# Kernel tuning notes

Measured on AMD Instinct MI355X. Metric: run time of the kernel, lower is better.

## Reference

```python
import jax, jax.numpy as jnp
import numpy as np

HIDDEN = 1024
HEADS = 16
HEAD_DIM = HIDDEN // HEADS
B, S = 2, 2048


def setup_inputs() -> dict:
    key = jax.random.key(0)
    ks = jax.random.split(key, 9)
    sc = 1.0 / np.sqrt(HIDDEN)
    return {
        "hidden_state": jax.random.normal(ks[0], (B, S, HIDDEN), dtype=jnp.float32),
        "wq": jax.random.normal(ks[1], (HIDDEN, HIDDEN), dtype=jnp.float32) * sc,
        "bq": jax.random.normal(ks[2], (HIDDEN,), dtype=jnp.float32) * 0.01,
        "wk": jax.random.normal(ks[3], (HIDDEN, HIDDEN), dtype=jnp.float32) * sc,
        "bk": jax.random.normal(ks[4], (HIDDEN,), dtype=jnp.float32) * 0.01,
        "wv": jax.random.normal(ks[5], (HIDDEN, HIDDEN), dtype=jnp.float32) * sc,
        "bv": jax.random.normal(ks[6], (HIDDEN,), dtype=jnp.float32) * 0.01,
        "wo": jax.random.normal(ks[7], (HIDDEN, HIDDEN), dtype=jnp.float32) * sc,
        "bo": jax.random.normal(ks[8], (HIDDEN,), dtype=jnp.float32) * 0.01,
    }


def reference(hidden_state, wq, bq, wk, bk, wv, bv, wo, bo):
    b, s, _ = hidden_state.shape

    def split_head(x):  # [B,S,H*D] -> [B,H,S,D]
        return x.reshape(b, s, HEADS, HEAD_DIM).transpose(0, 2, 1, 3)

    q = split_head(hidden_state @ wq + bq)
    k = split_head(hidden_state @ wk + bk)
    v = split_head(hidden_state @ wv + bv)

    # NOTE: original scales by sqrt(hidden_size), NOT sqrt(head_dim)
    scale = 1.0 / jnp.sqrt(jnp.float32(HIDDEN))
    scores = jnp.einsum("bhqd,bhkd->bhqk", q, k) * scale  # [B,H,S,S]
    probs = jax.nn.softmax(scores, axis=-1)
    out = jnp.einsum("bhqk,bhkd->bhqd", probs, v)  # [B,H,S,D]

    # Faithful to source: transpose(-1,-2) then view (this is the original's
    # layout, which differs from the conventional transpose(1,2) merge)
    out = out.transpose(0, 1, 3, 2).reshape(b, -1, HEADS * HEAD_DIM)
    return out @ wo + bo
```

## Files before the change

kernel.cpp:

```cpp
#include <hip/hip_runtime.h>
#include <stdint.h>


typedef unsigned short u16;
typedef __bf16 bf16x8 __attribute__((ext_vector_type(8)));
typedef u16 u16x8 __attribute__((ext_vector_type(8)));
typedef u16 u16x4 __attribute__((ext_vector_type(4)));
typedef float f32x4 __attribute__((ext_vector_type(4)));

#define DEV static __device__ __forceinline__

DEV bf16x8 as_bf16x8(u16x8 u) { union { u16x8 u; bf16x8 b; } c; c.u = u; return c.b; }
DEV u16 f2bf(float f) {
  uint32_t u = __float_as_uint(f);
  u += 0x7fffu + ((u >> 16) & 1u);
  return (u16)(u >> 16);
}
#if __has_builtin(__builtin_amdgcn_exp2f)
DEV float ex2(float x) { return __builtin_amdgcn_exp2f(x); }
#else
DEV float ex2(float x) { return exp2f(x); }
#endif

DEV void gll16(const u16* g, u16* lds) {
  __builtin_amdgcn_global_load_lds((const __attribute__((address_space(1))) void*)g,
                                   (__attribute__((address_space(3))) void*)lds,
                                   16, 0, 0);
}

__global__ __launch_bounds__(256) void prep_kernel(
    const float* __restrict__ hid, const float* __restrict__ w0,
    const float* __restrict__ w1, const float* __restrict__ w2,
    const float* __restrict__ w3, u16* __restrict__ Ah,
    u16* __restrict__ Wt) {
  __shared__ __align__(16) float T[64][68];
  int bid = blockIdx.x, t = threadIdx.x;
  if (bid < 2048) {
    int i = (bid * 256 + t) * 8;
    f32x4 a = *(const f32x4*)&hid[i];
    f32x4 b = *(const f32x4*)&hid[i + 4];
    u16x8 o;
#pragma unroll
    for (int j = 0; j < 4; ++j) { o[j] = f2bf(a[j]); o[j + 4] = f2bf(b[j]); }
    *(u16x8*)&Ah[i] = o;
    return;
  }
  int tb = bid - 2048;
  int z = tb >> 8, rem = tb & 255;
  const float* W = (z == 0) ? w0 : (z == 1) ? w1 : (z == 2) ? w2 : w3;
  u16* O = Wt + (size_t)z * 1024 * 1024;
  int r0 = (rem >> 4) * 64, c0 = (rem & 15) * 64;
  int i = t >> 2, js = (t & 3) * 16;
#pragma unroll
  for (int jj = 0; jj < 16; jj += 4)
    *(f32x4*)&T[i][js + jj] = *(const f32x4*)&W[(size_t)(r0 + i) * 1024 + c0 + js + jj];
  __syncthreads();
#pragma unroll
  for (int seg = 0; seg < 2; ++seg) {
    u16x8 v;
#pragma unroll
    for (int jj = 0; jj < 8; ++jj) v[jj] = f2bf(T[js + seg * 8 + jj][i]);
    *(u16x8*)&O[(size_t)(c0 + i) * 1024 + r0 + js + seg * 8] = v;
  }
}

DEV void gemm_body(const u16* __restrict__ A, const u16* __restrict__ Bt,
                   const float* __restrict__ bias, u16* __restrict__ C,
                   int mode, float scale) {
  __shared__ __align__(16) u16 As[2][128 * 32], Bs[2][128 * 32];
  int tid = threadIdx.x, lane = tid & 63, w = tid >> 6;
  int quad = lane >> 4, l15 = lane & 15;
  int m0 = blockIdx.x * 128, n0 = blockIdx.y * 128;
  int wm = w >> 1, wn = w & 1;
  f32x4 acc[4][4] = {};

  const int idx0 = tid, idx1 = 256 + tid;
  const int row0 = idx0 >> 2, c0g = ((idx0 & 3) ^ ((row0 >> 1) & 3)) * 8;
  const int row1 = idx1 >> 2, c1g = ((idx1 & 3) ^ ((row1 >> 1) & 3)) * 8;
  const u16* Ap0 = A + (size_t)(m0 + row0) * 1024 + c0g;
  const u16* Ap1 = A + (size_t)(m0 + row1) * 1024 + c1g;
  const u16* Bp0 = Bt + (size_t)(n0 + row0) * 1024 + c0g;
  const u16* Bp1 = Bt + (size_t)(n0 + row1) * 1024 + c1g;

  u16x8 ta0, ta1, tb0, tb1;
  ta0 = *(const u16x8*)Ap0;
  ta1 = *(const u16x8*)Ap1;
  tb0 = *(const u16x8*)Bp0;
  tb1 = *(const u16x8*)Bp1;
  *(u16x8*)&As[0][idx0 * 8] = ta0;
  *(u16x8*)&As[0][idx1 * 8] = ta1;
  *(u16x8*)&Bs[0][idx0 * 8] = tb0;
  *(u16x8*)&Bs[0][idx1 * 8] = tb1;
  __syncthreads();

  for (int k0 = 0; k0 < 1024; k0 += 32) {
    int cur = (k0 >> 5) & 1;
    if (k0 < 992) {
      ta0 = *(const u16x8*)(Ap0 + k0 + 32);
      ta1 = *(const u16x8*)(Ap1 + k0 + 32);
      tb0 = *(const u16x8*)(Bp0 + k0 + 32);
      tb1 = *(const u16x8*)(Bp1 + k0 + 32);
    }

    bf16x8 af[4], bfr[4];
#pragma unroll
    for (int mt = 0; mt < 4; ++mt) {
      int row = wm * 64 + mt * 16 + l15;
      af[mt] = as_bf16x8(*(const u16x8*)&As[cur][row * 32 + (quad ^ ((row >> 1) & 3)) * 8]);
    }
#pragma unroll
    for (int nt = 0; nt < 4; ++nt) {
      int row = wn * 64 + nt * 16 + l15;
      bfr[nt] = as_bf16x8(*(const u16x8*)&Bs[cur][row * 32 + (quad ^ ((row >> 1) & 3)) * 8]);
    }
    __builtin_amdgcn_s_setprio(1);
#pragma unroll
    for (int mt = 0; mt < 4; ++mt)
#pragma unroll
      for (int nt = 0; nt < 4; ++nt)
        acc[mt][nt] = __builtin_amdgcn_mfma_f32_16x16x32_bf16(af[mt], bfr[nt], acc[mt][nt], 0, 0, 0);
    __builtin_amdgcn_s_setprio(0);

    if (k0 < 992) {
      int nb = cur ^ 1;
      *(u16x8*)&As[nb][idx0 * 8] = ta0;
      *(u16x8*)&As[nb][idx1 * 8] = ta1;
      *(u16x8*)&Bs[nb][idx0 * 8] = tb0;
      *(u16x8*)&Bs[nb][idx1 * 8] = tb1;
    }
    __syncthreads();
  }

#pragma unroll
  for (int nt = 0; nt < 4; ++nt) {
    int n = n0 + wn * 64 + nt * 16 + l15;
    float bv = bias[n];
#pragma unroll
    for (int mt = 0; mt < 4; ++mt) {
      int mbase = m0 + wm * 64 + mt * 16 + quad * 4;
      if (mode == 2) {
        int b = mbase >> 11, s = mbase & 2047, h = n >> 6, d = n & 63;
        size_t base = (((size_t)(b * 16 + h)) * 64 + d) * 2048 + s;
        u16x4 pk;
#pragma unroll
        for (int r = 0; r < 4; ++r) pk[r] = f2bf((acc[mt][nt][r] + bv) * scale);
        *(u16x4*)&C[base] = pk;
      } else {
#pragma unroll
        for (int r = 0; r < 4; ++r) {
          int m = mbase + r;
          int b = m >> 11, s = m & 2047, h = n >> 6, d = n & 63;
          C[(((size_t)(b * 16 + h)) * 2048 + s) * 64 + d] =
              f2bf((acc[mt][nt][r] + bv) * scale);
        }
      }
    }
  }
}

__global__ __launch_bounds__(256) void qkv_gemm(
    const u16* __restrict__ A, const u16* __restrict__ Wt,
    const float* __restrict__ bq, const float* __restrict__ bk,
    const float* __restrict__ bv, u16* __restrict__ Qb, u16* __restrict__ Kb,
    u16* __restrict__ Vt) {
  int z = blockIdx.z;
  const u16* Bt = Wt + (size_t)z * 1024 * 1024;
  const float* bias = (z == 0) ? bq : (z == 1) ? bk : bv;
  u16* C = (z == 0) ? Qb : (z == 1) ? Kb : Vt;
  gemm_body(A, Bt, bias, C, (z == 2) ? 2 : 1, (z == 0) ? 0.045084220f : 1.0f);
}

__global__ __launch_bounds__(256) void out_gemm(
    const u16* __restrict__ A, const u16* __restrict__ Wt,
    const float* __restrict__ bo, float* __restrict__ C) {
  const u16* Bt = Wt + (size_t)3 * 1024 * 1024;
  __shared__ __align__(16) u16 As[2][64 * 32], Bs[2][128 * 32];
  int tid = threadIdx.x, lane = tid & 63, w = tid >> 6;
  int quad = lane >> 4, l15 = lane & 15;
  int m0 = blockIdx.x * 64, n0 = blockIdx.y * 128;
  f32x4 acc[4][2] = {};

  const int arow = tid >> 2, acg = ((tid & 3) ^ ((arow >> 1) & 3)) * 8;
  const int bidx0 = tid, bidx1 = 256 + tid;
  const int brow0 = bidx0 >> 2, bc0 = ((bidx0 & 3) ^ ((brow0 >> 1) & 3)) * 8;
  const int brow1 = bidx1 >> 2, bc1 = ((bidx1 & 3) ^ ((brow1 >> 1) & 3)) * 8;
  const u16* Ap = A + (size_t)(m0 + arow) * 1024 + acg;
  const u16* Bp0 = Bt + (size_t)(n0 + brow0) * 1024 + bc0;
  const u16* Bp1 = Bt + (size_t)(n0 + brow1) * 1024 + bc1;

  u16x8 ta, tb0, tb1;
  ta = *(const u16x8*)Ap;
  tb0 = *(const u16x8*)Bp0;
  tb1 = *(const u16x8*)Bp1;
  *(u16x8*)&As[0][tid * 8] = ta;
  *(u16x8*)&Bs[0][bidx0 * 8] = tb0;
  *(u16x8*)&Bs[0][bidx1 * 8] = tb1;
  __syncthreads();

  for (int k0 = 0; k0 < 1024; k0 += 32) {
    int cur = (k0 >> 5) & 1;
    if (k0 < 992) {
      ta = *(const u16x8*)(Ap + k0 + 32);
      tb0 = *(const u16x8*)(Bp0 + k0 + 32);
      tb1 = *(const u16x8*)(Bp1 + k0 + 32);
    }

    bf16x8 af[4], bfr[2];
#pragma unroll
    for (int mt = 0; mt < 4; ++mt) {
      int row = mt * 16 + l15;
      af[mt] = as_bf16x8(*(const u16x8*)&As[cur][row * 32 + (quad ^ ((row >> 1) & 3)) * 8]);
    }
#pragma unroll
    for (int nt = 0; nt < 2; ++nt) {
      int row = w * 32 + nt * 16 + l15;
      bfr[nt] = as_bf16x8(*(const u16x8*)&Bs[cur][row * 32 + (quad ^ ((row >> 1) & 3)) * 8]);
    }
    __builtin_amdgcn_s_setprio(1);
#pragma unroll
    for (int mt = 0; mt < 4; ++mt)
#pragma unroll
      for (int nt = 0; nt < 2; ++nt)
        acc[mt][nt] = __builtin_amdgcn_mfma_f32_16x16x32_bf16(af[mt], bfr[nt], acc[mt][nt], 0, 0, 0);
    __builtin_amdgcn_s_setprio(0);

    if (k0 < 992) {
      int nb = cur ^ 1;
      *(u16x8*)&As[nb][tid * 8] = ta;
      *(u16x8*)&Bs[nb][bidx0 * 8] = tb0;
      *(u16x8*)&Bs[nb][bidx1 * 8] = tb1;
    }
    __syncthreads();
  }

#pragma unroll
  for (int nt = 0; nt < 2; ++nt) {
    int n = n0 + w * 32 + nt * 16 + l15;
    float bv = bo[n];
#pragma unroll
    for (int mt = 0; mt < 4; ++mt) {
      int mbase = m0 + mt * 16 + quad * 4;
#pragma unroll
      for (int r = 0; r < 4; ++r)
        C[(size_t)(mbase + r) * 1024 + n] = acc[mt][nt][r] + bv;
    }
  }
}

#define PSTR 80
__global__ __launch_bounds__(256, 2) void attn_kernel(
    const u16* __restrict__ Qb, const u16* __restrict__ Kb,
    const u16* __restrict__ Vtb, u16* __restrict__ Otb) {
  __shared__ __align__(16) u16 Ks[2][64 * PSTR], Vs[2][64 * PSTR];
  int tid = threadIdx.x, lane = tid & 63, w = tid >> 6;
  int quad = lane >> 4, l15 = lane & 15;
  int bh = blockIdx.x, q0 = blockIdx.y * 128;
  const size_t baseQK = (size_t)bh * 2048 * 64;

  bf16x8 bq[2][2];
#pragma unroll
  for (int g = 0; g < 2; ++g) {
    int qrow = q0 + w * 32 + g * 16 + l15;
#pragma unroll
    for (int ks = 0; ks < 2; ++ks)
      bq[g][ks] = as_bf16x8(*(const u16x8*)&Qb[baseQK + (size_t)qrow * 64 + (ks * 4 + quad) * 8]);
  }

  bf16x8 av1;
  {
    u16x8 o1;
#pragma unroll
    for (int j = 0; j < 8; ++j) o1[j] = 0x3F80;
    av1 = as_bf16x8(o1);
  }

  f32x4 o[2][4] = {};
  f32x4 l_acc[2] = {};
  const int km = ((l15 & 12) << 1) | (l15 & 3);
  const int srow = tid >> 3, scs = tid & 7;
  const int srow2 = 32 + srow;

  u16x8 tk[2], tv[2];
  tk[0] = *(const u16x8*)&Kb[baseQK + (size_t)srow * 64 + scs * 8];
  tk[1] = *(const u16x8*)&Kb[baseQK + (size_t)srow2 * 64 + scs * 8];
  tv[0] = *(const u16x8*)&Vtb[baseQK + (size_t)srow * 2048 + scs * 8];
  tv[1] = *(const u16x8*)&Vtb[baseQK + (size_t)srow2 * 2048 + scs * 8];
  *(u16x8*)&Ks[0][srow * PSTR + scs * 8] = tk[0];
  *(u16x8*)&Ks[0][srow2 * PSTR + scs * 8] = tk[1];
  *(u16x8*)&Vs[0][srow * PSTR + scs * 8] = tv[0];
  *(u16x8*)&Vs[0][srow2 * PSTR + scs * 8] = tv[1];
  __syncthreads();

  for (int kv = 0; kv < 32; ++kv) {
    int cur = kv & 1;
    if (kv < 31) {
      tk[0] = *(const u16x8*)&Kb[baseQK + (size_t)((kv + 1) * 64 + srow) * 64 + scs * 8];
      tk[1] = *(const u16x8*)&Kb[baseQK + (size_t)((kv + 1) * 64 + srow2) * 64 + scs * 8];
      tv[0] = *(const u16x8*)&Vtb[baseQK + (size_t)srow * 2048 + (kv + 1) * 64 + scs * 8];
      tv[1] = *(const u16x8*)&Vtb[baseQK + (size_t)srow2 * 2048 + (kv + 1) * 64 + scs * 8];
    }

    f32x4 scA[2][2] = {}, scB[2][2] = {};
    __builtin_amdgcn_s_setprio(1);
#pragma unroll
    for (int ks = 0; ks < 2; ++ks)
#pragma unroll
      for (int mtg = 0; mtg < 2; ++mtg) {
        bf16x8 akA = as_bf16x8(*(const u16x8*)&Ks[cur][(mtg * 32 + km) * PSTR + (ks * 4 + quad) * 8]);
        bf16x8 akB = as_bf16x8(*(const u16x8*)&Ks[cur][(mtg * 32 + km + 4) * PSTR + (ks * 4 + quad) * 8]);
#pragma unroll
        for (int g = 0; g < 2; ++g) {
          scA[g][mtg] = __builtin_amdgcn_mfma_f32_16x16x32_bf16(akA, bq[g][ks], scA[g][mtg], 0, 0, 0);
          scB[g][mtg] = __builtin_amdgcn_mfma_f32_16x16x32_bf16(akB, bq[g][ks], scB[g][mtg], 0, 0, 0);
        }
      }
    __builtin_amdgcn_s_setprio(0);

    bf16x8 bp[2][2];
#pragma unroll
    for (int g = 0; g < 2; ++g)
#pragma unroll
      for (int mtg = 0; mtg < 2; ++mtg) {
        float pA0 = ex2(scA[g][mtg][0]), pA1 = ex2(scA[g][mtg][1]);
        float pA2 = ex2(scA[g][mtg][2]), pA3 = ex2(scA[g][mtg][3]);
        float pB0 = ex2(scB[g][mtg][0]), pB1 = ex2(scB[g][mtg][1]);
        float pB2 = ex2(scB[g][mtg][2]), pB3 = ex2(scB[g][mtg][3]);
        bp[g][mtg] = (bf16x8){(__bf16)pA0, (__bf16)pA1, (__bf16)pA2, (__bf16)pA3,
                              (__bf16)pB0, (__bf16)pB1, (__bf16)pB2, (__bf16)pB3};
        l_acc[g] = __builtin_amdgcn_mfma_f32_16x16x32_bf16(av1, bp[g][mtg], l_acc[g], 0, 0, 0);
      }

    __builtin_amdgcn_s_setprio(1);
#pragma unroll
    for (int mtg = 0; mtg < 2; ++mtg)
#pragma unroll
      for (int dt = 0; dt < 4; ++dt) {
        bf16x8 av = as_bf16x8(*(const u16x8*)&Vs[cur][(dt * 16 + l15) * PSTR + (mtg * 4 + quad) * 8]);
#pragma unroll
        for (int g = 0; g < 2; ++g)
          o[g][dt] = __builtin_amdgcn_mfma_f32_16x16x32_bf16(av, bp[g][mtg], o[g][dt], 0, 0, 0);
      }
    __builtin_amdgcn_s_setprio(0);

    if (kv < 31) {
      int nb = cur ^ 1;
      *(u16x8*)&Ks[nb][srow * PSTR + scs * 8] = tk[0];
      *(u16x8*)&Ks[nb][srow2 * PSTR + scs * 8] = tk[1];
      *(u16x8*)&Vs[nb][srow * PSTR + scs * 8] = tv[0];
      *(u16x8*)&Vs[nb][srow2 * PSTR + scs * 8] = tv[1];
    }
    __syncthreads();
  }

#pragma unroll
  for (int g = 0; g < 2; ++g) {
    float inv = 1.0f / l_acc[g][0];
#pragma unroll
    for (int dt = 0; dt < 4; ++dt)
#pragma unroll
      for (int r = 0; r < 4; ++r) {
        int d = dt * 16 + quad * 4 + r;
        Otb[(size_t)bh * 64 * 2048 + (size_t)d * 2048 + q0 + w * 32 + g * 16 + l15] =
            f2bf(o[g][dt][r] * inv);
      }
  }
}

extern "C" void kernel_launch(void* const* d_in, const int* in_sizes, int n_in,
                              void* d_out, int out_size, void* d_ws, size_t ws_size,
                              hipStream_t stream) {
  const float* hid = (const float*)d_in[0];
  const float* wq = (const float*)d_in[1];
  const float* bq = (const float*)d_in[2];
  const float* wk = (const float*)d_in[3];
  const float* bk = (const float*)d_in[4];
  const float* wv = (const float*)d_in[5];
  const float* bv = (const float*)d_in[6];
  const float* wo = (const float*)d_in[7];
  const float* bo = (const float*)d_in[8];

  u16* ws = (u16*)d_ws;
  const size_t MB2 = (size_t)1024 * 1024;
  u16* Wt  = ws;
  u16* Ah  = ws + 4 * MB2;
  u16* Qb  = ws + 8 * MB2;
  u16* Kb  = ws + 12 * MB2;
  u16* Vtb = ws + 16 * MB2;
  u16* Otb = Ah;

  prep_kernel<<<3072, 256, 0, stream>>>(hid, wq, wk, wv, wo, Ah, Wt);
  qkv_gemm<<<dim3(32, 8, 3), 256, 0, stream>>>(Ah, Wt, bq, bk, bv, Qb, Kb, Vtb);
  attn_kernel<<<dim3(32, 16), 256, 0, stream>>>(Qb, Kb, Vtb, Otb);
  out_gemm<<<dim3(64, 8), 256, 0, stream>>>(Otb, Wt, bo, (float*)d_out);
}
```

Before: 179.6 us.

## Fuse Q/K/V projections into one GEMM block sharing the A tile

The QKV GEMM now has each block compute a 128x64 tile for all three weight matrices at once, instead of launching a z-dimension of three separate 128x128 GEMMs. The A tile is loaded once per k-step and reused across the Q, K and V products, which cuts global and LDS traffic for the activations. In exchange the block keeps 96 accumulator vectors instead of 64, which raises register pressure, and the launch-bounds hint asks for two blocks per CU. The grid shrinks from 768 blocks to 512.

```diff
diff --git a/kernel.cpp b/kernel.cpp
--- a/kernel.cpp
+++ b/kernel.cpp
@@ -21,12 +21,6 @@
 #else
 DEV float ex2(float x) { return exp2f(x); }
 #endif
-
-DEV void gll16(const u16* g, u16* lds) {
-  __builtin_amdgcn_global_load_lds((const __attribute__((address_space(1))) void*)g,
-                                   (__attribute__((address_space(3))) void*)lds,
-                                   16, 0, 0);
-}
 
 __global__ __launch_bounds__(256) void prep_kernel(
     const float* __restrict__ hid, const float* __restrict__ w0,
@@ -64,33 +58,39 @@
   }
 }
 
-DEV void gemm_body(const u16* __restrict__ A, const u16* __restrict__ Bt,
-                   const float* __restrict__ bias, u16* __restrict__ C,
-                   int mode, float scale) {
-  __shared__ __align__(16) u16 As[2][128 * 32], Bs[2][128 * 32];
+__global__ __launch_bounds__(256, 2) void qkv_gemm(
+    const u16* __restrict__ A, const u16* __restrict__ Wt,
+    const float* __restrict__ bq, const float* __restrict__ bk,
+    const float* __restrict__ bv, u16* __restrict__ Qb, u16* __restrict__ Kb,
+    u16* __restrict__ Vt) {
+  __shared__ __align__(16) u16 As[2][128 * 32], Bs[2][3][64 * 32];
   int tid = threadIdx.x, lane = tid & 63, w = tid >> 6;
   int quad = lane >> 4, l15 = lane & 15;
-  int m0 = blockIdx.x * 128, n0 = blockIdx.y * 128;
+  int m0 = blockIdx.x * 128, n0 = blockIdx.y * 64;
   int wm = w >> 1, wn = w & 1;
-  f32x4 acc[4][4] = {};
+  f32x4 acc[3][4][2] = {};
 
   const int idx0 = tid, idx1 = 256 + tid;
-  const int row0 = idx0 >> 2, c0g = ((idx0 & 3) ^ ((row0 >> 1) & 3)) * 8;
-  const int row1 = idx1 >> 2, c1g = ((idx1 & 3) ^ ((row1 >> 1) & 3)) * 8;
-  const u16* Ap0 = A + (size_t)(m0 + row0) * 1024 + c0g;
-  const u16* Ap1 = A + (size_t)(m0 + row1) * 1024 + c1g;
-  const u16* Bp0 = Bt + (size_t)(n0 + row0) * 1024 + c0g;
-  const u16* Bp1 = Bt + (size_t)(n0 + row1) * 1024 + c1g;
-
-  u16x8 ta0, ta1, tb0, tb1;
+  const int arow0 = idx0 >> 2, ac0 = ((idx0 & 3) ^ ((arow0 >> 1) & 3)) * 8;
+  const int arow1 = idx1 >> 2, ac1 = ((idx1 & 3) ^ ((arow1 >> 1) & 3)) * 8;
+  const u16* Ap0 = A + (size_t)(m0 + arow0) * 1024 + ac0;
+  const u16* Ap1 = A + (size_t)(m0 + arow1) * 1024 + ac1;
+  const int brow = tid >> 2, bcg = ((tid & 3) ^ ((brow >> 1) & 3)) * 8;
+  const u16* Bp0 = Wt + (size_t)(n0 + brow) * 1024 + bcg;
+  const u16* Bp1 = Bp0 + (size_t)1024 * 1024;
+  const u16* Bp2 = Bp0 + (size_t)2 * 1024 * 1024;
+
+  u16x8 ta0, ta1, tb0, tb1, tb2;
   ta0 = *(const u16x8*)Ap0;
   ta1 = *(const u16x8*)Ap1;
   tb0 = *(const u16x8*)Bp0;
   tb1 = *(const u16x8*)Bp1;
+  tb2 = *(const u16x8*)Bp2;
   *(u16x8*)&As[0][idx0 * 8] = ta0;
   *(u16x8*)&As[0][idx1 * 8] = ta1;
-  *(u16x8*)&Bs[0][idx0 * 8] = tb0;
-  *(u16x8*)&Bs[0][idx1 * 8] = tb1;
+  *(u16x8*)&Bs[0][0][tid * 8] = tb0;
+  *(u16x8*)&Bs[0][1][tid * 8] = tb1;
+  *(u16x8*)&Bs[0][2][tid * 8] = tb2;
   __syncthreads();
 
   for (int k0 = 0; k0 < 1024; k0 += 32) {
@@ -100,74 +100,82 @@
       ta1 = *(const u16x8*)(Ap1 + k0 + 32);
       tb0 = *(const u16x8*)(Bp0 + k0 + 32);
       tb1 = *(const u16x8*)(Bp1 + k0 + 32);
-    }
-
-    bf16x8 af[4], bfr[4];
+      tb2 = *(const u16x8*)(Bp2 + k0 + 32);
+    }
+
+    bf16x8 af[4];
 #pragma unroll
     for (int mt = 0; mt < 4; ++mt) {
       int row = wm * 64 + mt * 16 + l15;
       af[mt] = as_bf16x8(*(const u16x8*)&As[cur][row * 32 + (quad ^ ((row >> 1) & 3)) * 8]);
     }
-#pragma unroll
-    for (int nt = 0; nt < 4; ++nt) {
-      int row = wn * 64 + nt * 16 + l15;
-      bfr[nt] = as_bf16x8(*(const u16x8*)&Bs[cur][row * 32 + (quad ^ ((row >> 1) & 3)) * 8]);
-    }
     __builtin_amdgcn_s_setprio(1);
 #pragma unroll
-    for (int mt = 0; mt < 4; ++mt)
-#pragma unroll
-      for (int nt = 0; nt < 4; ++nt)
-        acc[mt][nt] = __builtin_amdgcn_mfma_f32_16x16x32_bf16(af[mt], bfr[nt], acc[mt][nt], 0, 0, 0);
+    for (int z = 0; z < 3; ++z) {
+      bf16x8 bfr[2];
+#pragma unroll
+      for (int nt = 0; nt < 2; ++nt) {
+        int row = wn * 32 + nt * 16 + l15;
+        bfr[nt] = as_bf16x8(*(const u16x8*)&Bs[cur][z][row * 32 + (quad ^ ((row >> 1) & 3)) * 8]);
+      }
+#pragma unroll
+      for (int mt = 0; mt < 4; ++mt)
+#pragma unroll
+        for (int nt = 0; nt < 2; ++nt)
+          acc[z][mt][nt] = __builtin_amdgcn_mfma_f32_16x16x32_bf16(af[mt], bfr[nt], acc[z][mt][nt], 0, 0, 0);
+    }
     __builtin_amdgcn_s_setprio(0);
 
     if (k0 < 992) {
       int nb = cur ^ 1;
       *(u16x8*)&As[nb][idx0 * 8] = ta0;
       *(u16x8*)&As[nb][idx1 * 8] = ta1;
-      *(u16x8*)&Bs[nb][idx0 * 8] = tb0;
-      *(u16x8*)&Bs[nb][idx1 * 8] = tb1;
+      *(u16x8*)&Bs[nb][0][tid * 8] = tb0;
+      *(u16x8*)&Bs[nb][1][tid * 8] = tb1;
+      *(u16x8*)&Bs[nb][2][tid * 8] = tb2;
     }
     __syncthreads();
   }
 
 #pragma unroll
-  for (int nt = 0; nt < 4; ++nt) {
-    int n = n0 + wn * 64 + nt * 16 + l15;
-    float bv = bias[n];
+  for (int z = 0; z < 2; ++z) {
+    const float* bias = (z == 0) ? bq : bk;
+    u16* C = (z == 0) ? Qb : Kb;
+    float scale = (z == 0) ? 0.045084220f : 1.0f;
+#pragma unroll
+    for (int nt = 0; nt < 2; ++nt) {
+      int n = n0 + wn * 32 + nt * 16 + l15;
+      float bb = bias[n];
+      int h = n >> 6, d = n & 63;
+#pragma unroll
+      for (int mt = 0; mt < 4; ++mt) {
+        int mbase = m0 + wm * 64 + mt * 16 + quad * 4;
+#pragma unroll
+        for (int r = 0; r < 4; ++r) {
+          int m = mbase + r;
+          int b = m >> 11, s = m & 2047;
+          C[(((size_t)(b * 16 + h)) * 2048 + s) * 64 + d] =
+              f2bf((acc[z][mt][nt][r] + bb) * scale);
+        }
+      }
+    }
+  }
+#pragma unroll
+  for (int nt = 0; nt < 2; ++nt) {
+    int n = n0 + wn * 32 + nt * 16 + l15;
+    float bb = bv[n];
+    int h = n >> 6, d = n & 63;
 #pragma unroll
     for (int mt = 0; mt < 4; ++mt) {
       int mbase = m0 + wm * 64 + mt * 16 + quad * 4;
-      if (mode == 2) {
-        int b = mbase >> 11, s = mbase & 2047, h = n >> 6, d = n & 63;
-        size_t base = (((size_t)(b * 16 + h)) * 64 + d) * 2048 + s;
-        u16x4 pk;
-#pragma unroll
-        for (int r = 0; r < 4; ++r) pk[r] = f2bf((acc[mt][nt][r] + bv) * scale);
-        *(u16x4*)&C[base] = pk;
-      } else {
-#pragma unroll
-        for (int r = 0; r < 4; ++r) {
-          int m = mbase + r;
-          int b = m >> 11, s = m & 2047, h = n >> 6, d = n & 63;
-          C[(((size_t)(b * 16 + h)) * 2048 + s) * 64 + d] =
-              f2bf((acc[mt][nt][r] + bv) * scale);
-        }
-      }
-    }
-  }
-}
-
-__global__ __launch_bounds__(256) void qkv_gemm(
-    const u16* __restrict__ A, const u16* __restrict__ Wt,
-    const float* __restrict__ bq, const float* __restrict__ bk,
-    const float* __restrict__ bv, u16* __restrict__ Qb, u16* __restrict__ Kb,
-    u16* __restrict__ Vt) {
-  int z = blockIdx.z;
-  const u16* Bt = Wt + (size_t)z * 1024 * 1024;
-  const float* bias = (z == 0) ? bq : (z == 1) ? bk : bv;
-  u16* C = (z == 0) ? Qb : (z == 1) ? Kb : Vt;
-  gemm_body(A, Bt, bias, C, (z == 2) ? 2 : 1, (z == 0) ? 0.045084220f : 1.0f);
+      int b = mbase >> 11, s = mbase & 2047;
+      size_t base = (((size_t)(b * 16 + h)) * 64 + d) * 2048 + s;
+      u16x4 pk;
+#pragma unroll
+      for (int r = 0; r < 4; ++r) pk[r] = f2bf(acc[2][mt][nt][r] + bb);
+      *(u16x4*)&Vt[base] = pk;
+    }
+  }
 }
 
 __global__ __launch_bounds__(256) void out_gemm(
@@ -389,7 +397,7 @@
   u16* Otb = Ah;
 
   prep_kernel<<<3072, 256, 0, stream>>>(hid, wq, wk, wv, wo, Ah, Wt);
-  qkv_gemm<<<dim3(32, 8, 3), 256, 0, stream>>>(Ah, Wt, bq, bk, bv, Qb, Kb, Vtb);
+  qkv_gemm<<<dim3(32, 16), 256, 0, stream>>>(Ah, Wt, bq, bk, bv, Qb, Kb, Vtb);
   attn_kernel<<<dim3(32, 16), 256, 0, stream>>>(Qb, Kb, Vtb, Otb);
   out_gemm<<<dim3(64, 8), 256, 0, stream>>>(Otb, Wt, bo, (float*)d_out);
 }
```

Result: no change. 178.6 us (median of 2 runs) (-0.6%).
